# Kernel tuning notes

Measured on AMD Instinct MI355X. Metric: run time of the kernel, lower is better.

Reference implementation:

```python
import jax, jax.numpy as jnp
import numpy as np


def reference(x, edge_index, edge_attr, W, b):
    """PyG GCNConv: out = D^{-1/2} (A + I) D^{-1/2} X W + b.

    x: [N, Din] node features
    edge_index: [2, E] int (row=source, col=target)
    edge_attr: [E] edge weights
    W: [Din, Dout], b: [Dout]
    """
    N = x.shape[0]
    # add self-loops with weight 1 (PyG fill_value=1.0)
    loop = jnp.arange(N, dtype=edge_index.dtype)
    row = jnp.concatenate([edge_index[0], loop])
    col = jnp.concatenate([edge_index[1], loop])
    w = jnp.concatenate([edge_attr, jnp.ones((N,), dtype=edge_attr.dtype)])

    # symmetric normalization: norm_e = d[row]^-1/2 * w_e * d[col]^-1/2
    deg = jax.ops.segment_sum(w, col, num_segments=N)
    dis = jnp.where(deg > 0, jax.lax.rsqrt(jnp.where(deg > 0, deg, 1.0)), 0.0)
    norm = dis[row] * w * dis[col]

    # linear projection first (Din == Dout, cheaper either way), then
    # gather-scale-scatter aggregation at targets
    h = x @ W                                   # [N, Dout]
    msg = h[row] * norm[:, None]                # [E+N, Dout]
    out = jax.ops.segment_sum(msg, col, num_segments=N)  # [N, Dout]
    return out + b


def setup_inputs() -> dict:
    key = jax.random.key(0)
    k1, k2, k3, k4 = jax.random.split(key, 4)
    N, E, Din, Dout = 100000, 1600000, 128, 128
    x = jax.random.normal(k1, (N, Din), dtype=jnp.float32)
    edge_index = jax.random.randint(k2, (2, E), 0, N, dtype=jnp.int64)
    edge_attr = jax.random.uniform(k3, (E,), dtype=jnp.float32)
    # Glorot init like PyG Linear default
    W = jax.random.normal(k4, (Din, Dout), dtype=jnp.float32) * (1.0 / np.sqrt(Din))
    b = jnp.zeros((Dout,), dtype=jnp.float32)
    return {"x": x, "edge_index": edge_index, "edge_attr": edge_attr, "W": W, "b": b}
```

## Files before the change

kernel.cpp:

```cpp
#include <hip/hip_runtime.h>


#define ELEMS_PER_SCAN_BLOCK 4096
#define SCAN_SHIFT 12
#define CHUNK 2048
#define NCMAX 800

typedef __attribute__((ext_vector_type(8))) short short8;
typedef __attribute__((ext_vector_type(4))) float f32x4;

__device__ inline unsigned short f2bf(float f) {
    unsigned u = __float_as_uint(f);
    u += 0x7fffu + ((u >> 16) & 1u);
    return (unsigned short)(u >> 16);
}
__device__ inline float bf_lo(unsigned u) { return __uint_as_float(u << 16); }
__device__ inline float bf_hi(unsigned u) { return __uint_as_float(u & 0xffff0000u); }

__global__ __launch_bounds__(256) void k_hist(const int* __restrict__ col,
                                              const float* __restrict__ W,
                                              int* __restrict__ histg,
                                              unsigned short* __restrict__ Wtg,
                                              int E, int NC, int NBLK) {
    __shared__ int lh[1024];
    int t = threadIdx.x, blk = blockIdx.x;
    if (blk < 64) {
        int n = blk * 2 + (t >> 7);
        int k = t & 127;
        Wtg[n * 128 + k] = f2bf(W[k * 128 + n]);
    }
    for (int i = t; i < 1024; i += 256) lh[i] = 0;
    __syncthreads();
    int base = blk * CHUNK;
    #pragma unroll
    for (int i = 0; i < CHUNK / 256; ++i) {
        int e = base + i * 256 + t;
        if (e < E) atomicAdd(&lh[col[e] >> 7], 1);
    }
    __syncthreads();
    for (int b = t; b < NC; b += 256) histg[b * NBLK + blk] = lh[b];
}

__device__ inline int wave_incl_scan(int x, int lane) {
    #pragma unroll
    for (int d = 1; d < 64; d <<= 1) {
        int y = __shfl_up(x, d, 64);
        if (lane >= d) x += y;
    }
    return x;
}

__global__ void k_scan1(const int* __restrict__ in, int* __restrict__ out,
                        int* __restrict__ bsum, int M) {
    __shared__ int wsum[4];
    __shared__ int woff[4];
    int t = threadIdx.x, lane = t & 63, wid = t >> 6;
    int base = blockIdx.x * ELEMS_PER_SCAN_BLOCK + t * 16;
    int v[16];
    #pragma unroll
    for (int i = 0; i < 16; ++i) v[i] = (base + i < M) ? in[base + i] : 0;
    int run = 0;
    #pragma unroll
    for (int i = 0; i < 16; ++i) { int x = v[i]; v[i] = run; run += x; }
    int incl = wave_incl_scan(run, lane);
    int excl = incl - run;
    if (lane == 63) wsum[wid] = incl;
    __syncthreads();
    if (t == 0) {
        int r = 0;
        #pragma unroll
        for (int w = 0; w < 4; ++w) { int s = wsum[w]; woff[w] = r; r += s; }
        bsum[blockIdx.x] = r;
    }
    __syncthreads();
    int off = woff[wid] + excl;
    #pragma unroll
    for (int i = 0; i < 16; ++i)
        if (base + i < M) out[base + i] = v[i] + off;
}

__global__ void k_scan2(const int* __restrict__ bsum, int* __restrict__ boff, int NB) {
    __shared__ int wsum[4];
    __shared__ int woff[4];
    int t = threadIdx.x, lane = t & 63, wid = t >> 6;
    int x = (t < NB) ? bsum[t] : 0;
    int incl = wave_incl_scan(x, lane);
    int excl = incl - x;
    if (lane == 63) wsum[wid] = incl;
    __syncthreads();
    if (t == 0) {
        int r = 0;
        #pragma unroll
        for (int w = 0; w < 4; ++w) { int s = wsum[w]; woff[w] = r; r += s; }
    }
    __syncthreads();
    if (t < NB) boff[t] = woff[wid] + excl;
}

__global__ __launch_bounds__(256) void k_place(const int* __restrict__ row,
                                               const int* __restrict__ col,
                                               const float* __restrict__ wgt,
                                               const int* __restrict__ histg,
                                               const int* __restrict__ boff,
                                               int2* __restrict__ srw,
                                               int E, int NC, int NBLK) {
    __shared__ struct { int lcnt[NCMAX]; int gadj[NCMAX]; int2 stage[CHUNK];
                        int sdst[CHUNK]; int wsum[4]; int woff[4]; } sp;
    int t = threadIdx.x, blk = blockIdx.x;
    int lane = t & 63, wid = t >> 6;
    int base = blk * CHUNK;
    int nE = min(CHUNK, E - base);
    for (int b = t; b < NCMAX; b += 256) sp.lcnt[b] = 0;
    __syncthreads();
    #pragma unroll
    for (int i = 0; i < CHUNK / 256; ++i) {
        int e = base + i * 256 + t;
        if (e < E) atomicAdd(&sp.lcnt[col[e] >> 7], 1);
    }
    __syncthreads();
    int c4[4];
    int sum = 0;
    #pragma unroll
    for (int i = 0; i < 4; ++i) {
        int idx = t * 4 + i;
        int v = (idx < NCMAX) ? sp.lcnt[idx] : 0;
        c4[i] = sum; sum += v;
    }
    int incl = wave_incl_scan(sum, lane);
    int excl = incl - sum;
    if (lane == 63) sp.wsum[wid] = incl;
    __syncthreads();
    if (t == 0) {
        int r = 0;
        #pragma unroll
        for (int w = 0; w < 4; ++w) { int s = sp.wsum[w]; sp.woff[w] = r; r += s; }
    }
    __syncthreads();
    int tb = sp.woff[wid] + excl;
    __syncthreads();
    #pragma unroll
    for (int i = 0; i < 4; ++i) {
        int idx = t * 4 + i;
        if (idx < NCMAX) {
            int b0 = tb + c4[i];
            int gb = 0;
            if (idx < NC) {
                int g = idx * NBLK + blk;
                gb = histg[g] + boff[g >> SCAN_SHIFT];
            }
            sp.gadj[idx] = gb - b0;
            sp.lcnt[idx] = b0;
        }
    }
    __syncthreads();
    #pragma unroll
    for (int i = 0; i < CHUNK / 256; ++i) {
        int e = base + i * 256 + t;
        if (e < E) {
            int c = col[e];
            int slot = atomicAdd(&sp.lcnt[c >> 7], 1);
            sp.stage[slot] = make_int2(((c & 127) << 17) | row[e], __float_as_int(wgt[e]));
            sp.sdst[slot] = sp.gadj[c >> 7] + slot;
        }
    }
    __syncthreads();
    for (int s_ = t; s_ < nE; s_ += 256) {
        srw[sp.sdst[s_]] = sp.stage[s_];
    }
}

__global__ __launch_bounds__(256) void k_fine(const int* __restrict__ histg,
                                              const int* __restrict__ boff,
                                              const int2* __restrict__ srw,
                                              int* __restrict__ rowptr,
                                              float* __restrict__ dis,
                                              int2* __restrict__ spack,
                                              int E, int N, int NC, int NBLK) {
    __shared__ struct { int2 sbuf[3072]; int cnt128[128]; float degf[128];
                        int cur128[128]; int wtot[2]; } sf;
    int t = threadIdx.x, b = blockIdx.x;
    int nb = b << 7;
    int g0 = b * NBLK;
    int start = histg[g0] + boff[g0 >> SCAN_SHIFT];
    int end;
    if (b == NC - 1) end = E;
    else {
        int g1 = (b + 1) * NBLK;
        end = histg[g1] + boff[g1 >> SCAN_SHIFT];
    }
    int cnt = end - start;
    int NL = min(cnt, 3072);
    if (t < 128) { sf.cnt128[t] = 0; sf.degf[t] = 1.0f; }
    __syncthreads();
    for (int j = t; j < cnt; j += 256) {
        int2 s = srw[start + j];
        if (j < NL) sf.sbuf[j] = s;
        int c = s.x >> 17;
        atomicAdd(&sf.cnt128[c], 1);
        atomicAdd(&sf.degf[c], __int_as_float(s.y));
    }
    __syncthreads();
    int v = 0, incl = 0;
    if (t < 128) {
        v = sf.cnt128[t];
        incl = wave_incl_scan(v, t & 63);
        if ((t & 63) == 63) sf.wtot[t >> 6] = incl;
    }
    __syncthreads();
    if (t < 128) {
        int excl = incl - v + ((t >= 64) ? sf.wtot[0] : 0);
        int p = start + excl;
        sf.cur128[t] = p;
        int n = nb + t;
        if (n < N) {
            rowptr[n] = p;
            dis[n] = rsqrtf(sf.degf[t]);
        }
    }
    if (t == 0 && b == NC - 1) rowptr[N] = E;
    __syncthreads();
    for (int j = t; j < cnt; j += 256) {
        int2 s = (j < NL) ? sf.sbuf[j] : srw[start + j];
        int c = s.x >> 17;
        int pos = atomicAdd(&sf.cur128[c], 1);
        spack[pos] = make_int2(s.x & 0x1FFFF, s.y);
    }
}

__global__ __launch_bounds__(256) void k_gemm(const float* __restrict__ x,
                                              const unsigned short* __restrict__ Wtg,
                                              const float* __restrict__ dis,
                                              unsigned short* __restrict__ h, int N) {
    __shared__ struct { short Xs[64][72]; short Ws[128][72]; } sm;
    int t = threadIdx.x;
    int lane = t & 63, wid = t >> 6;
    int row0 = blockIdx.x * 64;
    int q = lane >> 4;
    int m = lane & 15;
    f32x4 acc[8];
    #pragma unroll
    for (int tde = 0; tde < 8; ++tde) acc[tde] = (f32x4){0.f, 0.f, 0.f, 0.f};

    #pragma unroll
    for (int kh = 0; kh < 2; ++kh) {
        {
            int r = t >> 2;
            int kf = (t & 3) * 16;
            int gr = row0 + r;
            const float4* src = (const float4*)(x + (size_t)gr * 128 + kh * 64 + kf);
            float4 a0 = make_float4(0.f, 0.f, 0.f, 0.f), a1 = a0, a2 = a0, a3 = a0;
            if (gr < N) { a0 = src[0]; a1 = src[1]; a2 = src[2]; a3 = src[3]; }
            short8 p0, p1;
            p0[0] = (short)f2bf(a0.x); p0[1] = (short)f2bf(a0.y);
            p0[2] = (short)f2bf(a0.z); p0[3] = (short)f2bf(a0.w);
            p0[4] = (short)f2bf(a1.x); p0[5] = (short)f2bf(a1.y);
            p0[6] = (short)f2bf(a1.z); p0[7] = (short)f2bf(a1.w);
            p1[0] = (short)f2bf(a2.x); p1[1] = (short)f2bf(a2.y);
            p1[2] = (short)f2bf(a2.z); p1[3] = (short)f2bf(a2.w);
            p1[4] = (short)f2bf(a3.x); p1[5] = (short)f2bf(a3.y);
            p1[6] = (short)f2bf(a3.z); p1[7] = (short)f2bf(a3.w);
            *(short8*)&sm.Xs[r][kf]     = p0;
            *(short8*)&sm.Xs[r][kf + 8] = p1;
        }
        {
            int n = t >> 1;
            int off = (t & 1) * 32;
            const short* wsrc = (const short*)Wtg + n * 128 + kh * 64 + off;
            #pragma unroll
            for (int i = 0; i < 4; ++i)
                *(short8*)&sm.Ws[n][off + 8 * i] = *(const short8*)(wsrc + 8 * i);
        }
        __syncthreads();
        #pragma unroll
        for (int kc = 0; kc < 64; kc += 32) {
            short8 af = *(const short8*)&sm.Xs[wid * 16 + m][kc + q * 8];
            #pragma unroll
            for (int tde = 0; tde < 8; ++tde) {
                short8 bf = *(const short8*)&sm.Ws[tde * 16 + m][kc + q * 8];
                acc[tde] = __builtin_amdgcn_mfma_f32_16x16x32_bf16(af, bf, acc[tde], 0, 0, 0);
            }
        }
        __syncthreads();
    }
    #pragma unroll
    for (int r = 0; r < 4; ++r) {
        int grow = row0 + wid * 16 + q * 4 + r;
        if (grow < N) {
            float dn = dis[grow];
            #pragma unroll
            for (int tde = 0; tde < 8; ++tde)
                h[(size_t)grow * 128 + tde * 16 + m] = f2bf(dn * acc[tde][r]);
        }
    }
}

__global__ __launch_bounds__(256) void k_gather(const unsigned int* __restrict__ hb,
                                                const float* __restrict__ dis,
                                                const int* __restrict__ rowptr,
                                                const long* __restrict__ spackl,
                                                const float* __restrict__ bias,
                                                float* __restrict__ out, int N) {
    int gid = blockIdx.x * blockDim.x + threadIdx.x;
    int node = gid >> 6;
    int lane = gid & 63;
    if (node >= N) return;
    node = __builtin_amdgcn_readfirstlane(node);

    float dn = dis[node];
    unsigned u = hb[(size_t)node * 64 + lane];
    float2 acc;
    acc.x = bf_lo(u);
    acc.y = bf_hi(u);

    int jb = rowptr[node], je = rowptr[node + 1];
    int j = jb;
    for (; j + 8 <= je; j += 8) {
        long q0 = __builtin_nontemporal_load(spackl + j);
        long q1 = __builtin_nontemporal_load(spackl + j + 1);
        long q2 = __builtin_nontemporal_load(spackl + j + 2);
        long q3 = __builtin_nontemporal_load(spackl + j + 3);
        long q4 = __builtin_nontemporal_load(spackl + j + 4);
        long q5 = __builtin_nontemporal_load(spackl + j + 5);
        long q6 = __builtin_nontemporal_load(spackl + j + 6);
        long q7 = __builtin_nontemporal_load(spackl + j + 7);
        int r0 = __builtin_amdgcn_readfirstlane((int)q0);
        int r1 = __builtin_amdgcn_readfirstlane((int)q1);
        int r2 = __builtin_amdgcn_readfirstlane((int)q2);
        int r3 = __builtin_amdgcn_readfirstlane((int)q3);
        int r4 = __builtin_amdgcn_readfirstlane((int)q4);
        int r5 = __builtin_amdgcn_readfirstlane((int)q5);
        int r6 = __builtin_amdgcn_readfirstlane((int)q6);
        int r7 = __builtin_amdgcn_readfirstlane((int)q7);
        unsigned u0 = hb[(size_t)r0 * 64 + lane];
        unsigned u1 = hb[(size_t)r1 * 64 + lane];
        unsigned u2 = hb[(size_t)r2 * 64 + lane];
        unsigned u3 = hb[(size_t)r3 * 64 + lane];
        unsigned u4 = hb[(size_t)r4 * 64 + lane];
        unsigned u5 = hb[(size_t)r5 * 64 + lane];
        unsigned u6 = hb[(size_t)r6 * 64 + lane];
        unsigned u7 = hb[(size_t)r7 * 64 + lane];
        float a0 = __uint_as_float((unsigned)((unsigned long)q0 >> 32));
        float a1 = __uint_as_float((unsigned)((unsigned long)q1 >> 32));
        float a2 = __uint_as_float((unsigned)((unsigned long)q2 >> 32));
        float a3 = __uint_as_float((unsigned)((unsigned long)q3 >> 32));
        float a4 = __uint_as_float((unsigned)((unsigned long)q4 >> 32));
        float a5 = __uint_as_float((unsigned)((unsigned long)q5 >> 32));
        float a6 = __uint_as_float((unsigned)((unsigned long)q6 >> 32));
        float a7 = __uint_as_float((unsigned)((unsigned long)q7 >> 32));
        acc.x = fmaf(a0, bf_lo(u0), acc.x); acc.y = fmaf(a0, bf_hi(u0), acc.y);
        acc.x = fmaf(a1, bf_lo(u1), acc.x); acc.y = fmaf(a1, bf_hi(u1), acc.y);
        acc.x = fmaf(a2, bf_lo(u2), acc.x); acc.y = fmaf(a2, bf_hi(u2), acc.y);
        acc.x = fmaf(a3, bf_lo(u3), acc.x); acc.y = fmaf(a3, bf_hi(u3), acc.y);
        acc.x = fmaf(a4, bf_lo(u4), acc.x); acc.y = fmaf(a4, bf_hi(u4), acc.y);
        acc.x = fmaf(a5, bf_lo(u5), acc.x); acc.y = fmaf(a5, bf_hi(u5), acc.y);
        acc.x = fmaf(a6, bf_lo(u6), acc.x); acc.y = fmaf(a6, bf_hi(u6), acc.y);
        acc.x = fmaf(a7, bf_lo(u7), acc.x); acc.y = fmaf(a7, bf_hi(u7), acc.y);
    }
    for (; j < je; ++j) {
        long q = __builtin_nontemporal_load(spackl + j);
        int r = __builtin_amdgcn_readfirstlane((int)q);
        unsigned uu = hb[(size_t)r * 64 + lane];
        float a = __uint_as_float((unsigned)((unsigned long)q >> 32));
        acc.x = fmaf(a, bf_lo(uu), acc.x);
        acc.y = fmaf(a, bf_hi(uu), acc.y);
    }

    int c0 = lane * 2;
    float2 bv = *(const float2*)(bias + c0);
    float2 o;
    o.x = bv.x + dn * acc.x;
    o.y = bv.y + dn * acc.y;
    union { float2 f; double d; } cvt;
    cvt.f = o;
    __builtin_nontemporal_store(cvt.d, (double*)(out + (size_t)node * 128 + c0));
}

extern "C" void kernel_launch(void* const* d_in, const int* in_sizes, int n_in,
                              void* d_out, int out_size, void* d_ws, size_t ws_size,
                              hipStream_t stream) {
    const float* x     = (const float*)d_in[0];
    const int*   eidx  = (const int*)d_in[1];
    const float* eattr = (const float*)d_in[2];
    const float* W     = (const float*)d_in[3];
    const float* bias  = (const float*)d_in[4];
    int N = in_sizes[0] / 128;
    int E = in_sizes[2];
    const int* row = eidx;
    const int* col = eidx + E;

    int NC = (N + 127) >> 7;
    int NBLK = (E + CHUNK - 1) / CHUNK;

    char* p = (char*)d_ws;
    auto carve = [&](size_t bytes) {
        char* q = p;
        p += (bytes + 255) & ~(size_t)255;
        return q;
    };
    unsigned short* h   = (unsigned short*)carve((size_t)N * 128 * sizeof(unsigned short));
    unsigned short* Wtg = (unsigned short*)carve(128 * 128 * sizeof(unsigned short));
    float* dis    = (float*)carve((size_t)N * sizeof(float));
    int*   rowptr = (int*)carve((size_t)(N + 1) * sizeof(int));
    int*   histg  = (int*)carve((size_t)NC * NBLK * sizeof(int));
    int2*  srw    = (int2*)carve((size_t)E * sizeof(int2));
    int2*  spack  = (int2*)carve((size_t)E * sizeof(int2));
    int*   bsum   = (int*)carve(256 * sizeof(int));
    int*   boff   = (int*)carve(256 * sizeof(int));

    int M = NC * NBLK;
    int NBs = (M + ELEMS_PER_SCAN_BLOCK - 1) / ELEMS_PER_SCAN_BLOCK;
    int GB = (N + 63) / 64;

    k_hist<<<NBLK, 256, 0, stream>>>(col, W, histg, Wtg, E, NC, NBLK);
    k_scan1<<<NBs, 256, 0, stream>>>(histg, histg, bsum, M);
    k_scan2<<<1, 256, 0, stream>>>(bsum, boff, NBs);
    k_place<<<NBLK, 256, 0, stream>>>(row, col, eattr, histg, boff, srw, E, NC, NBLK);
    k_fine<<<NC, 256, 0, stream>>>(histg, boff, srw, rowptr, dis, spack, E, N, NC, NBLK);
    k_gemm<<<GB, 256, 0, stream>>>(x, Wtg, dis, h, N);
    {
        size_t threads = (size_t)N * 64;
        int blocks = (int)((threads + 255) / 256);
        k_gather<<<blocks, 256, 0, stream>>>((const unsigned int*)h, dis, rowptr,
                                             (const long*)spack, bias, (float*)d_out, N);
    }
}
```

Baseline: 248.9 us.

## Replace histogram-and-scan bucketing with atomic reservation into fixed-capacity buckets

Drops the separate histogram kernel and the two-level global scan. Instead, each placement block reserves space per coarse bucket with a global atomicAdd into fixed-capacity slots (CAP per bucket). A small single-block scan over the bucket counts then gives output offsets for the fine sort. This removes one full pass over the column indices and several launches. The cost is a larger staging buffer and silent truncation of any bucket that exceeds CAP, which random inputs are unlikely to hit but skewed graphs could. Edge order within a bucket is also no longer deterministic.

```diff
diff --git a/kernel.cpp b/kernel.cpp
--- a/kernel.cpp
+++ b/kernel.cpp
@@ -1,10 +1,9 @@
 #include <hip/hip_runtime.h>
 
 
-#define ELEMS_PER_SCAN_BLOCK 4096
-#define SCAN_SHIFT 12
 #define CHUNK 2048
 #define NCMAX 800
+#define CAP 3072
 
 typedef __attribute__((ext_vector_type(8))) short short8;
 typedef __attribute__((ext_vector_type(4))) float f32x4;
@@ -17,97 +16,32 @@
 __device__ inline float bf_lo(unsigned u) { return __uint_as_float(u << 16); }
 __device__ inline float bf_hi(unsigned u) { return __uint_as_float(u & 0xffff0000u); }
 
-__global__ __launch_bounds__(256) void k_hist(const int* __restrict__ col,
-                                              const float* __restrict__ W,
-                                              int* __restrict__ histg,
-                                              unsigned short* __restrict__ Wtg,
-                                              int E, int NC, int NBLK) {
-    __shared__ int lh[1024];
+__device__ inline int wave_incl_scan(int x, int lane) {
+    #pragma unroll
+    for (int d = 1; d < 64; d <<= 1) {
+        int y = __shfl_up(x, d, 64);
+        if (lane >= d) x += y;
+    }
+    return x;
+}
+
+__global__ __launch_bounds__(256) void k_place(const int* __restrict__ row,
+                                               const int* __restrict__ col,
+                                               const float* __restrict__ wgt,
+                                               const float* __restrict__ W,
+                                               unsigned short* __restrict__ Wtg,
+                                               int* __restrict__ gcur,
+                                               int2* __restrict__ srw,
+                                               int E, int NC) {
+    __shared__ struct { int lcnt[NCMAX]; int gadj[NCMAX]; int2 stage[CHUNK];
+                        int sdst[CHUNK]; int wsum[4]; int woff[4]; } sp;
     int t = threadIdx.x, blk = blockIdx.x;
+    int lane = t & 63, wid = t >> 6;
     if (blk < 64) {
         int n = blk * 2 + (t >> 7);
         int k = t & 127;
         Wtg[n * 128 + k] = f2bf(W[k * 128 + n]);
     }
-    for (int i = t; i < 1024; i += 256) lh[i] = 0;
-    __syncthreads();
-    int base = blk * CHUNK;
-    #pragma unroll
-    for (int i = 0; i < CHUNK / 256; ++i) {
-        int e = base + i * 256 + t;
-        if (e < E) atomicAdd(&lh[col[e] >> 7], 1);
-    }
-    __syncthreads();
-    for (int b = t; b < NC; b += 256) histg[b * NBLK + blk] = lh[b];
-}
-
-__device__ inline int wave_incl_scan(int x, int lane) {
-    #pragma unroll
-    for (int d = 1; d < 64; d <<= 1) {
-        int y = __shfl_up(x, d, 64);
-        if (lane >= d) x += y;
-    }
-    return x;
-}
-
-__global__ void k_scan1(const int* __restrict__ in, int* __restrict__ out,
-                        int* __restrict__ bsum, int M) {
-    __shared__ int wsum[4];
-    __shared__ int woff[4];
-    int t = threadIdx.x, lane = t & 63, wid = t >> 6;
-    int base = blockIdx.x * ELEMS_PER_SCAN_BLOCK + t * 16;
-    int v[16];
-    #pragma unroll
-    for (int i = 0; i < 16; ++i) v[i] = (base + i < M) ? in[base + i] : 0;
-    int run = 0;
-    #pragma unroll
-    for (int i = 0; i < 16; ++i) { int x = v[i]; v[i] = run; run += x; }
-    int incl = wave_incl_scan(run, lane);
-    int excl = incl - run;
-    if (lane == 63) wsum[wid] = incl;
-    __syncthreads();
-    if (t == 0) {
-        int r = 0;
-        #pragma unroll
-        for (int w = 0; w < 4; ++w) { int s = wsum[w]; woff[w] = r; r += s; }
-        bsum[blockIdx.x] = r;
-    }
-    __syncthreads();
-    int off = woff[wid] + excl;
-    #pragma unroll
-    for (int i = 0; i < 16; ++i)
-        if (base + i < M) out[base + i] = v[i] + off;
-}
-
-__global__ void k_scan2(const int* __restrict__ bsum, int* __restrict__ boff, int NB) {
-    __shared__ int wsum[4];
-    __shared__ int woff[4];
-    int t = threadIdx.x, lane = t & 63, wid = t >> 6;
-    int x = (t < NB) ? bsum[t] : 0;
-    int incl = wave_incl_scan(x, lane);
-    int excl = incl - x;
-    if (lane == 63) wsum[wid] = incl;
-    __syncthreads();
-    if (t == 0) {
-        int r = 0;
-        #pragma unroll
-        for (int w = 0; w < 4; ++w) { int s = wsum[w]; woff[w] = r; r += s; }
-    }
-    __syncthreads();
-    if (t < NB) boff[t] = woff[wid] + excl;
-}
-
-__global__ __launch_bounds__(256) void k_place(const int* __restrict__ row,
-                                               const int* __restrict__ col,
-                                               const float* __restrict__ wgt,
-                                               const int* __restrict__ histg,
-                                               const int* __restrict__ boff,
-                                               int2* __restrict__ srw,
-                                               int E, int NC, int NBLK) {
-    __shared__ struct { int lcnt[NCMAX]; int gadj[NCMAX]; int2 stage[CHUNK];
-                        int sdst[CHUNK]; int wsum[4]; int woff[4]; } sp;
-    int t = threadIdx.x, blk = blockIdx.x;
-    int lane = t & 63, wid = t >> 6;
     int base = blk * CHUNK;
     int nE = min(CHUNK, E - base);
     for (int b = t; b < NCMAX; b += 256) sp.lcnt[b] = 0;
@@ -118,12 +52,13 @@
         if (e < E) atomicAdd(&sp.lcnt[col[e] >> 7], 1);
     }
     __syncthreads();
-    int c4[4];
+    int c4[4], cv[4];
     int sum = 0;
     #pragma unroll
     for (int i = 0; i < 4; ++i) {
         int idx = t * 4 + i;
         int v = (idx < NCMAX) ? sp.lcnt[idx] : 0;
+        cv[i] = v;
         c4[i] = sum; sum += v;
     }
     int incl = wave_incl_scan(sum, lane);
@@ -144,11 +79,8 @@
         if (idx < NCMAX) {
             int b0 = tb + c4[i];
             int gb = 0;
-            if (idx < NC) {
-                int g = idx * NBLK + blk;
-                gb = histg[g] + boff[g >> SCAN_SHIFT];
-            }
-            sp.gadj[idx] = gb - b0;
+            if (idx < NC && cv[i] > 0) gb = atomicAdd(&gcur[idx], cv[i]);
+            sp.gadj[idx] = idx * CAP + gb - b0;
             sp.lcnt[idx] = b0;
         }
     }
@@ -164,36 +96,63 @@
         }
     }
     __syncthreads();
+    int lim = NC * CAP;
     for (int s_ = t; s_ < nE; s_ += 256) {
-        srw[sp.sdst[s_]] = sp.stage[s_];
-    }
-}
-
-__global__ __launch_bounds__(256) void k_fine(const int* __restrict__ histg,
-                                              const int* __restrict__ boff,
+        int d = sp.sdst[s_];
+        if (d < lim) srw[d] = sp.stage[s_];
+    }
+}
+
+__global__ void k_bscan(const int* __restrict__ gcur, int* __restrict__ bstart, int NC) {
+    __shared__ int wsum[4];
+    __shared__ int woff[4];
+    int t = threadIdx.x, lane = t & 63, wid = t >> 6;
+    int c4[4];
+    int sum = 0;
+    #pragma unroll
+    for (int i = 0; i < 4; ++i) {
+        int idx = t * 4 + i;
+        int v = (idx < NC) ? gcur[idx] : 0;
+        c4[i] = sum; sum += v;
+    }
+    int incl = wave_incl_scan(sum, lane);
+    int excl = incl - sum;
+    if (lane == 63) wsum[wid] = incl;
+    __syncthreads();
+    if (t == 0) {
+        int r = 0;
+        #pragma unroll
+        for (int w = 0; w < 4; ++w) { int s = wsum[w]; woff[w] = r; r += s; }
+    }
+    __syncthreads();
+    int tb = woff[wid] + excl;
+    #pragma unroll
+    for (int i = 0; i < 4; ++i) {
+        int idx = t * 4 + i;
+        if (idx < NC) bstart[idx] = tb + c4[i];
+    }
+}
+
+__global__ __launch_bounds__(256) void k_fine(const int* __restrict__ gcur,
+                                              const int* __restrict__ bstart,
                                               const int2* __restrict__ srw,
                                               int* __restrict__ rowptr,
                                               float* __restrict__ dis,
                                               int2* __restrict__ spack,
-                                              int E, int N, int NC, int NBLK) {
+                                              int E, int N, int NC) {
     __shared__ struct { int2 sbuf[3072]; int cnt128[128]; float degf[128];
                         int cur128[128]; int wtot[2]; } sf;
     int t = threadIdx.x, b = blockIdx.x;
     int nb = b << 7;
-    int g0 = b * NBLK;
-    int start = histg[g0] + boff[g0 >> SCAN_SHIFT];
-    int end;
-    if (b == NC - 1) end = E;
-    else {
-        int g1 = (b + 1) * NBLK;
-        end = histg[g1] + boff[g1 >> SCAN_SHIFT];
-    }
-    int cnt = end - start;
+    int cnt = gcur[b];
+    if (cnt > CAP) cnt = CAP;
+    int in_base = b * CAP;
+    int out_base = bstart[b];
     int NL = min(cnt, 3072);
     if (t < 128) { sf.cnt128[t] = 0; sf.degf[t] = 1.0f; }
     __syncthreads();
     for (int j = t; j < cnt; j += 256) {
-        int2 s = srw[start + j];
+        int2 s = srw[in_base + j];
         if (j < NL) sf.sbuf[j] = s;
         int c = s.x >> 17;
         atomicAdd(&sf.cnt128[c], 1);
@@ -209,7 +168,7 @@
     __syncthreads();
     if (t < 128) {
         int excl = incl - v + ((t >= 64) ? sf.wtot[0] : 0);
-        int p = start + excl;
+        int p = out_base + excl;
         sf.cur128[t] = p;
         int n = nb + t;
         if (n < N) {
@@ -217,10 +176,10 @@
             dis[n] = rsqrtf(sf.degf[t]);
         }
     }
-    if (t == 0 && b == NC - 1) rowptr[N] = E;
+    if (t == 0 && b == NC - 1) rowptr[N] = out_base + cnt;
     __syncthreads();
     for (int j = t; j < cnt; j += 256) {
-        int2 s = (j < NL) ? sf.sbuf[j] : srw[start + j];
+        int2 s = (j < NL) ? sf.sbuf[j] : srw[in_base + j];
         int c = s.x >> 17;
         int pos = atomicAdd(&sf.cur128[c], 1);
         spack[pos] = make_int2(s.x & 0x1FFFF, s.y);
@@ -401,21 +360,17 @@
     unsigned short* Wtg = (unsigned short*)carve(128 * 128 * sizeof(unsigned short));
     float* dis    = (float*)carve((size_t)N * sizeof(float));
     int*   rowptr = (int*)carve((size_t)(N + 1) * sizeof(int));
-    int*   histg  = (int*)carve((size_t)NC * NBLK * sizeof(int));
-    int2*  srw    = (int2*)carve((size_t)E * sizeof(int2));
+    int2*  srw    = (int2*)carve(((size_t)NC * CAP + CAP) * sizeof(int2));
     int2*  spack  = (int2*)carve((size_t)E * sizeof(int2));
-    int*   bsum   = (int*)carve(256 * sizeof(int));
-    int*   boff   = (int*)carve(256 * sizeof(int));
-
-    int M = NC * NBLK;
-    int NBs = (M + ELEMS_PER_SCAN_BLOCK - 1) / ELEMS_PER_SCAN_BLOCK;
+    int*   gcur   = (int*)carve((size_t)NCMAX * sizeof(int));
+    int*   bstart = (int*)carve((size_t)NCMAX * sizeof(int));
+
     int GB = (N + 63) / 64;
 
-    k_hist<<<NBLK, 256, 0, stream>>>(col, W, histg, Wtg, E, NC, NBLK);
-    k_scan1<<<NBs, 256, 0, stream>>>(histg, histg, bsum, M);
-    k_scan2<<<1, 256, 0, stream>>>(bsum, boff, NBs);
-    k_place<<<NBLK, 256, 0, stream>>>(row, col, eattr, histg, boff, srw, E, NC, NBLK);
-    k_fine<<<NC, 256, 0, stream>>>(histg, boff, srw, rowptr, dis, spack, E, N, NC, NBLK);
+    hipMemsetAsync(gcur, 0, (size_t)NCMAX * sizeof(int), stream);
+    k_place<<<NBLK, 256, 0, stream>>>(row, col, eattr, W, Wtg, gcur, srw, E, NC);
+    k_bscan<<<1, 256, 0, stream>>>(gcur, bstart, NC);
+    k_fine<<<NC, 256, 0, stream>>>(gcur, bstart, srw, rowptr, dis, spack, E, N, NC);
     k_gemm<<<GB, 256, 0, stream>>>(x, Wtg, dis, h, N);
     {
         size_t threads = (size_t)N * 64;
```

After: 290.8 us. 1.17x slower.

## Store block histograms row-major and transpose via LDS tiles for coalesced access

Applied to the files above, without the earlier changes.

k_hist now writes each block's coarse-bucket histogram contiguously (block-major) instead of strided column writes. Two new tiled-transpose kernels convert it to bucket-major for the scan and convert the scanned offsets back to block-major, so k_place reads both its counts and its global offsets contiguously. This also lets k_place skip its second pass over col that recounted the local histogram. In exchange it adds two kernel launches and extra round trips of the histogram arrays through memory.

```diff
diff --git a/kernel.cpp b/kernel.cpp
--- a/kernel.cpp
+++ b/kernel.cpp
@@ -4,7 +4,7 @@
 #define ELEMS_PER_SCAN_BLOCK 4096
 #define SCAN_SHIFT 12
 #define CHUNK 2048
-#define NCMAX 800
+#define NCP 800
 
 typedef __attribute__((ext_vector_type(8))) short short8;
 typedef __attribute__((ext_vector_type(4))) float f32x4;
@@ -17,11 +17,20 @@
 __device__ inline float bf_lo(unsigned u) { return __uint_as_float(u << 16); }
 __device__ inline float bf_hi(unsigned u) { return __uint_as_float(u & 0xffff0000u); }
 
+__device__ inline int wave_incl_scan(int x, int lane) {
+    #pragma unroll
+    for (int d = 1; d < 64; d <<= 1) {
+        int y = __shfl_up(x, d, 64);
+        if (lane >= d) x += y;
+    }
+    return x;
+}
+
 __global__ __launch_bounds__(256) void k_hist(const int* __restrict__ col,
                                               const float* __restrict__ W,
-                                              int* __restrict__ histg,
+                                              int* __restrict__ histB,
                                               unsigned short* __restrict__ Wtg,
-                                              int E, int NC, int NBLK) {
+                                              int E, int NBLK) {
     __shared__ int lh[1024];
     int t = threadIdx.x, blk = blockIdx.x;
     if (blk < 64) {
@@ -38,16 +47,28 @@
         if (e < E) atomicAdd(&lh[col[e] >> 7], 1);
     }
     __syncthreads();
-    for (int b = t; b < NC; b += 256) histg[b * NBLK + blk] = lh[b];
-}
-
-__device__ inline int wave_incl_scan(int x, int lane) {
-    #pragma unroll
-    for (int d = 1; d < 64; d <<= 1) {
-        int y = __shfl_up(x, d, 64);
-        if (lane >= d) x += y;
-    }
-    return x;
+    for (int b = t; b < NCP; b += 256) histB[blk * NCP + b] = lh[b];
+}
+
+__global__ __launch_bounds__(256) void k_tr(const int* __restrict__ histB,
+                                            int* __restrict__ histT,
+                                            int NC, int NBLK, int TX) {
+    __shared__ int tl[64][65];
+    int t = threadIdx.x;
+    int ti = blockIdx.x % TX;
+    int tj = blockIdx.x / TX;
+    int k0 = ti * 64, b0 = tj * 64;
+    for (int i = t; i < 4096; i += 256) {
+        int r = i >> 6, c = i & 63;
+        int gb = k0 + r, bb = b0 + c;
+        tl[r][c] = (gb < NBLK && bb < NCP) ? histB[gb * NCP + bb] : 0;
+    }
+    __syncthreads();
+    for (int i = t; i < 4096; i += 256) {
+        int r = i >> 6, c = i & 63;
+        int bb = b0 + r, gb = k0 + c;
+        if (bb < NC && gb < NBLK) histT[bb * NBLK + gb] = tl[c][r];
+    }
 }
 
 __global__ void k_scan1(const int* __restrict__ in, int* __restrict__ out,
@@ -97,33 +118,54 @@
     if (t < NB) boff[t] = woff[wid] + excl;
 }
 
+__global__ __launch_bounds__(256) void k_tr2(const int* __restrict__ histT,
+                                             const int* __restrict__ boff,
+                                             int* __restrict__ scanB,
+                                             int NC, int NBLK, int TX) {
+    __shared__ int tl[64][65];
+    int t = threadIdx.x;
+    int ti = blockIdx.x % TX;
+    int tj = blockIdx.x / TX;
+    int k0 = ti * 64, b0 = tj * 64;
+    for (int i = t; i < 4096; i += 256) {
+        int r = i >> 6, c = i & 63;
+        int bb = b0 + r, gb = k0 + c;
+        int v = 0;
+        if (bb < NC && gb < NBLK) {
+            int g = bb * NBLK + gb;
+            v = histT[g] + boff[g >> SCAN_SHIFT];
+        }
+        tl[r][c] = v;
+    }
+    __syncthreads();
+    for (int i = t; i < 4096; i += 256) {
+        int r = i >> 6, c = i & 63;
+        int gb = k0 + r, bb = b0 + c;
+        if (gb < NBLK && bb < NCP) scanB[gb * NCP + bb] = tl[c][r];
+    }
+}
+
 __global__ __launch_bounds__(256) void k_place(const int* __restrict__ row,
                                                const int* __restrict__ col,
                                                const float* __restrict__ wgt,
-                                               const int* __restrict__ histg,
-                                               const int* __restrict__ boff,
+                                               const int* __restrict__ histB,
+                                               const int* __restrict__ scanB,
                                                int2* __restrict__ srw,
-                                               int E, int NC, int NBLK) {
-    __shared__ struct { int lcnt[NCMAX]; int gadj[NCMAX]; int2 stage[CHUNK];
+                                               int E, int NC) {
+    __shared__ struct { int lcnt[NCP]; int gadj[NCP]; int2 stage[CHUNK];
                         int sdst[CHUNK]; int wsum[4]; int woff[4]; } sp;
     int t = threadIdx.x, blk = blockIdx.x;
     int lane = t & 63, wid = t >> 6;
     int base = blk * CHUNK;
     int nE = min(CHUNK, E - base);
-    for (int b = t; b < NCMAX; b += 256) sp.lcnt[b] = 0;
-    __syncthreads();
-    #pragma unroll
-    for (int i = 0; i < CHUNK / 256; ++i) {
-        int e = base + i * 256 + t;
-        if (e < E) atomicAdd(&sp.lcnt[col[e] >> 7], 1);
-    }
-    __syncthreads();
-    int c4[4];
+    int c4[4], cv[4];
     int sum = 0;
     #pragma unroll
     for (int i = 0; i < 4; ++i) {
         int idx = t * 4 + i;
-        int v = (idx < NCMAX) ? sp.lcnt[idx] : 0;
+        int v = histB[blk * NCP + idx];
+        if (idx >= NCP) v = 0;
+        cv[i] = v;
         c4[i] = sum; sum += v;
     }
     int incl = wave_incl_scan(sum, lane);
@@ -137,17 +179,12 @@
     }
     __syncthreads();
     int tb = sp.woff[wid] + excl;
-    __syncthreads();
     #pragma unroll
     for (int i = 0; i < 4; ++i) {
         int idx = t * 4 + i;
-        if (idx < NCMAX) {
+        if (idx < NCP) {
             int b0 = tb + c4[i];
-            int gb = 0;
-            if (idx < NC) {
-                int g = idx * NBLK + blk;
-                gb = histg[g] + boff[g >> SCAN_SHIFT];
-            }
+            int gb = (idx < NC) ? scanB[blk * NCP + idx] : 0;
             sp.gadj[idx] = gb - b0;
             sp.lcnt[idx] = b0;
         }
@@ -169,7 +206,7 @@
     }
 }
 
-__global__ __launch_bounds__(256) void k_fine(const int* __restrict__ histg,
+__global__ __launch_bounds__(256) void k_fine(const int* __restrict__ histT,
                                               const int* __restrict__ boff,
                                               const int2* __restrict__ srw,
                                               int* __restrict__ rowptr,
@@ -181,12 +218,12 @@
     int t = threadIdx.x, b = blockIdx.x;
     int nb = b << 7;
     int g0 = b * NBLK;
-    int start = histg[g0] + boff[g0 >> SCAN_SHIFT];
+    int start = histT[g0] + boff[g0 >> SCAN_SHIFT];
     int end;
     if (b == NC - 1) end = E;
     else {
         int g1 = (b + 1) * NBLK;
-        end = histg[g1] + boff[g1 >> SCAN_SHIFT];
+        end = histT[g1] + boff[g1 >> SCAN_SHIFT];
     }
     int cnt = end - start;
     int NL = min(cnt, 3072);
@@ -401,7 +438,9 @@
     unsigned short* Wtg = (unsigned short*)carve(128 * 128 * sizeof(unsigned short));
     float* dis    = (float*)carve((size_t)N * sizeof(float));
     int*   rowptr = (int*)carve((size_t)(N + 1) * sizeof(int));
-    int*   histg  = (int*)carve((size_t)NC * NBLK * sizeof(int));
+    int*   histB  = (int*)carve((size_t)NBLK * NCP * sizeof(int));
+    int*   histT  = (int*)carve((size_t)NC * NBLK * sizeof(int));
+    int*   scanB  = (int*)carve((size_t)NBLK * NCP * sizeof(int));
     int2*  srw    = (int2*)carve((size_t)E * sizeof(int2));
     int2*  spack  = (int2*)carve((size_t)E * sizeof(int2));
     int*   bsum   = (int*)carve(256 * sizeof(int));
@@ -410,12 +449,16 @@
     int M = NC * NBLK;
     int NBs = (M + ELEMS_PER_SCAN_BLOCK - 1) / ELEMS_PER_SCAN_BLOCK;
     int GB = (N + 63) / 64;
-
-    k_hist<<<NBLK, 256, 0, stream>>>(col, W, histg, Wtg, E, NC, NBLK);
-    k_scan1<<<NBs, 256, 0, stream>>>(histg, histg, bsum, M);
+    int TX = (NBLK + 63) / 64;
+    int TY = (NC + 63) / 64;
+
+    k_hist<<<NBLK, 256, 0, stream>>>(col, W, histB, Wtg, E, NBLK);
+    k_tr<<<TX * TY, 256, 0, stream>>>(histB, histT, NC, NBLK, TX);
+    k_scan1<<<NBs, 256, 0, stream>>>(histT, histT, bsum, M);
     k_scan2<<<1, 256, 0, stream>>>(bsum, boff, NBs);
-    k_place<<<NBLK, 256, 0, stream>>>(row, col, eattr, histg, boff, srw, E, NC, NBLK);
-    k_fine<<<NC, 256, 0, stream>>>(histg, boff, srw, rowptr, dis, spack, E, N, NC, NBLK);
+    k_tr2<<<TX * TY, 256, 0, stream>>>(histT, boff, scanB, NC, NBLK, TX);
+    k_place<<<NBLK, 256, 0, stream>>>(row, col, eattr, histB, scanB, srw, E, NC);
+    k_fine<<<NC, 256, 0, stream>>>(histT, boff, srw, rowptr, dis, spack, E, N, NC, NBLK);
     k_gemm<<<GB, 256, 0, stream>>>(x, Wtg, dis, h, N);
     {
         size_t threads = (size_t)N * 64;
```

New measurement: 259.7 us. 1.04x slower.
